# Kernel tuning notes

Hardware: AMD Instinct MI355X
Metric: run time of the kernel (lower is better)

## Reference

```python
import jax, jax.numpy as jnp
import numpy as np


def setup_inputs() -> dict:
    key = jax.random.key(0)
    k1, k2 = jax.random.split(key)
    B, N, M, D = 8, 4096, 4096, 3
    return {
        "input": jax.random.normal(k1, (B, N, D), dtype=jnp.float32),
        "target": jax.random.normal(k2, (B, M, D), dtype=jnp.float32),
    }


def reference(input, target):
    x2 = jnp.sum(input * input, axis=-1)          # [B, N]
    y2 = jnp.sum(target * target, axis=-1)        # [B, M]
    xy = jnp.einsum("bnd,bmd->bnm", input, target)  # [B, N, M]
    sqdist = x2[:, :, None] + y2[:, None, :] - 2.0 * xy
    sqdist = jnp.maximum(sqdist, 0.0)  # clamp numerical negatives
    sqdist1 = jnp.min(sqdist, axis=2)  # nearest target for each input point [B, N]
    sqdist2 = jnp.min(sqdist, axis=1)  # nearest input for each target point [B, M]
    return jnp.mean(sqdist1) + jnp.mean(sqdist2)
```

## Files before the change

### kernel.cpp

```cpp
#include <hip/hip_runtime.h>
#include <math.h>

#define BATCH 8
#define NPTS  4096
#define TPB   256
#define NCC   4
#define CHUNK (NPTS / NCC)
#define ROWS  256
#define NRC   (NPTS / ROWS)
#define WROWS 64

typedef __bf16 bf16x8 __attribute__((ext_vector_type(8)));
typedef float  f32x16 __attribute__((ext_vector_type(16)));

__global__ __launch_bounds__(TPB) void chamfer_mfma_kernel(
    const float* __restrict__ input,
    const float* __restrict__ target,
    float* __restrict__ part)
{
  const int dir = blockIdx.z, b = blockIdx.y;
  const int rc = blockIdx.x & (NRC - 1);
  const int cc = blockIdx.x >> 4;

  const float* __restrict__ qp = (dir ? target : input) + (size_t)b * NPTS * 3;
  const float* __restrict__ cp = (dir ? input  : target) + (size_t)b * NPTS * 3;

  __shared__ bf16x8 sB[2][CHUNK];
  __shared__ bf16x8 sA[2][ROWS];

  {
    const int c0 = cc * CHUNK + (int)threadIdx.x * 4;
    const float4* __restrict__ cv = (const float4*)(cp + 3 * c0);
    const float4 f0 = cv[0], f1 = cv[1], f2 = cv[2];
    float xs[4] = { f0.x, f0.w, f1.z, f2.y };
    float ys[4] = { f0.y, f1.x, f1.w, f2.z };
    float zs[4] = { f0.z, f1.y, f2.x, f2.w };
    #pragma unroll
    for (int j = 0; j < 4; ++j) {
      const float mx = -2.f * xs[j], my = -2.f * ys[j], mz = -2.f * zs[j];
      const __bf16 hx = (__bf16)mx, hy = (__bf16)my, hz = (__bf16)mz;
      const __bf16 lx = (__bf16)(mx - (float)hx);
      const __bf16 ly = (__bf16)(my - (float)hy);
      const __bf16 lz = (__bf16)(mz - (float)hz);
      const float y2 = fmaf(xs[j], xs[j], fmaf(ys[j], ys[j], zs[j] * zs[j]));
      const __bf16 h2 = (__bf16)y2, l2 = (__bf16)(y2 - (float)h2);
      const __bf16 z0 = (__bf16)0.f;
      bf16x8 v0, v1;
      v0[0]=hx; v0[1]=hy; v0[2]=hz; v0[3]=lx; v0[4]=ly; v0[5]=lz; v0[6]=z0; v0[7]=z0;
      v1[0]=hx; v1[1]=hy; v1[2]=hz; v1[3]=h2; v1[4]=l2; v1[5]=z0; v1[6]=z0; v1[7]=z0;
      sB[0][threadIdx.x * 4 + j] = v0;
      sB[1][threadIdx.x * 4 + j] = v1;
    }
  }
  {
    const int r = rc * ROWS + (int)threadIdx.x;
    const float qx = qp[3*r], qy = qp[3*r+1], qz = qp[3*r+2];
    const __bf16 hx = (__bf16)qx, hy = (__bf16)qy, hz = (__bf16)qz;
    const __bf16 lx = (__bf16)(qx - (float)hx);
    const __bf16 ly = (__bf16)(qy - (float)hy);
    const __bf16 lz = (__bf16)(qz - (float)hz);
    const __bf16 z0 = (__bf16)0.f, o1 = (__bf16)1.f;
    bf16x8 v0, v1;
    v0[0]=hx; v0[1]=hy; v0[2]=hz; v0[3]=hx; v0[4]=hy; v0[5]=hz; v0[6]=z0; v0[7]=z0;
    v1[0]=lx; v1[1]=ly; v1[2]=lz; v1[3]=o1; v1[4]=o1; v1[5]=z0; v1[6]=z0; v1[7]=z0;
    sA[0][threadIdx.x] = v0;
    sA[1][threadIdx.x] = v1;
  }
  __syncthreads();

  const int lane = (int)threadIdx.x & 63;
  const int wave = (int)threadIdx.x >> 6;
  const int half = lane >> 5;
  const int l31  = lane & 31;

  const bf16x8 a0 = sA[half][wave * WROWS + l31];
  const bf16x8 a1 = sA[half][wave * WROWS + 32 + l31];

  float rm0[16], rm1[16];
  #pragma unroll
  for (int i = 0; i < 16; ++i) { rm0[i] = 3.4e38f; rm1[i] = 3.4e38f; }

  f32x16 zacc;
  #pragma unroll
  for (int i = 0; i < 16; ++i) zacc[i] = 0.f;

  #pragma unroll 2
  for (int m = 0; m < CHUNK / 32; ++m) {
    const bf16x8 bf = sB[half][m * 32 + l31];
    const f32x16 d0 = __builtin_amdgcn_mfma_f32_32x32x16_bf16(a0, bf, zacc, 0, 0, 0);
    const f32x16 d1 = __builtin_amdgcn_mfma_f32_32x32x16_bf16(a1, bf, zacc, 0, 0, 0);
    #pragma unroll
    for (int i = 0; i < 16; ++i) {
      rm0[i] = fminf(rm0[i], d0[i]);
      rm1[i] = fminf(rm1[i], d1[i]);
    }
  }

  float* __restrict__ po = part +
      (((size_t)(dir * BATCH + b) * NCC + cc) * NPTS) + rc * ROWS + wave * WROWS;
  #pragma unroll
  for (int r = 0; r < 16; ++r) {
    float v0 = rm0[r], v1 = rm1[r];
    #pragma unroll
    for (int mk = 1; mk < 32; mk <<= 1) {
      v0 = fminf(v0, __shfl_xor(v0, mk, 64));
      v1 = fminf(v1, __shfl_xor(v1, mk, 64));
    }
    if (l31 == 0) {
      const int row = (r & 3) + 8 * (r >> 2) + 4 * half;
      po[row]      = v0;
      po[row + 32] = v1;
    }
  }
}

__global__ __launch_bounds__(TPB) void chamfer_reduce_kernel(
    const float* __restrict__ part,
    const float* __restrict__ input,
    const float* __restrict__ target,
    float* __restrict__ out)
{
  const int i = (blockIdx.x * TPB + (int)threadIdx.x) * 4;
  const int g = i >> 12;
  const int q = i & (NPTS - 1);
  const int dir = g >> 3, b = g & 7;

  const float* __restrict__ p = part + ((size_t)g * NCC) * NPTS + q;
  float4 mn = *(const float4*)p;
  #pragma unroll
  for (int cc = 1; cc < NCC; ++cc) {
    const float4 t = *(const float4*)(p + (size_t)cc * NPTS);
    mn.x = fminf(mn.x, t.x); mn.y = fminf(mn.y, t.y);
    mn.z = fminf(mn.z, t.z); mn.w = fminf(mn.w, t.w);
  }
  const float* __restrict__ qp =
      (dir ? target : input) + (size_t)b * NPTS * 3 + 3 * q;
  const float4* __restrict__ qv = (const float4*)qp;
  const float4 a = qv[0], c = qv[1], e = qv[2];
  const float x20 = fmaf(a.x, a.x, fmaf(a.y, a.y, a.z * a.z));
  const float x21 = fmaf(a.w, a.w, fmaf(c.x, c.x, c.y * c.y));
  const float x22 = fmaf(c.z, c.z, fmaf(c.w, c.w, e.x * e.x));
  const float x23 = fmaf(e.y, e.y, fmaf(e.z, e.z, e.w * e.w));

  float s = fmaxf(mn.x + x20, 0.f) + fmaxf(mn.y + x21, 0.f) +
            fmaxf(mn.z + x22, 0.f) + fmaxf(mn.w + x23, 0.f);
  #pragma unroll
  for (int off = 32; off > 0; off >>= 1)
    s += __shfl_down(s, off, 64);

  __shared__ float wsum[TPB / 64];
  if ((threadIdx.x & 63) == 0) wsum[threadIdx.x >> 6] = s;
  __syncthreads();
  if (threadIdx.x == 0) {
    const float t = wsum[0] + wsum[1] + wsum[2] + wsum[3];
    atomicAdd(out, t * (1.0f / (float)(BATCH * NPTS)));
  }
}

extern "C" void kernel_launch(void* const* d_in, const int* in_sizes, int n_in,
                              void* d_out, int out_size, void* d_ws, size_t ws_size,
                              hipStream_t stream) {
  const float* input  = (const float*)d_in[0];
  const float* target = (const float*)d_in[1];
  float* out  = (float*)d_out;
  float* part = (float*)d_ws;

  hipMemsetAsync(out, 0, sizeof(float), stream);

  dim3 grid1(NRC * NCC, BATCH, 2);
  chamfer_mfma_kernel<<<grid1, dim3(TPB), 0, stream>>>(input, target, part);

  dim3 grid2((2 * BATCH * NPTS) / (TPB * 4));
  chamfer_reduce_kernel<<<grid2, dim3(TPB), 0, stream>>>(part, input, target, out);
}
```

Measured before the change: 75.33 us.

## Replace shuffle row-min with swizzled LDS transpose and fold norm+clamp into MFMA kernel

```diff
diff --git a/kernel.cpp b/kernel.cpp
--- a/kernel.cpp
+++ b/kernel.cpp
@@ -8,7 +8,6 @@
 #define CHUNK (NPTS / NCC)
 #define ROWS  256
 #define NRC   (NPTS / ROWS)
-#define WROWS 64
 
 typedef __bf16 bf16x8 __attribute__((ext_vector_type(8)));
 typedef float  f32x16 __attribute__((ext_vector_type(16)));
@@ -52,9 +51,10 @@
       sB[1][threadIdx.x * 4 + j] = v1;
     }
   }
+  float qx, qy, qz;
   {
     const int r = rc * ROWS + (int)threadIdx.x;
-    const float qx = qp[3*r], qy = qp[3*r+1], qz = qp[3*r+2];
+    qx = qp[3*r]; qy = qp[3*r+1]; qz = qp[3*r+2];
     const __bf16 hx = (__bf16)qx, hy = (__bf16)qy, hz = (__bf16)qz;
     const __bf16 lx = (__bf16)(qx - (float)hx);
     const __bf16 ly = (__bf16)(qy - (float)hy);
@@ -73,8 +73,8 @@
   const int half = lane >> 5;
   const int l31  = lane & 31;
 
-  const bf16x8 a0 = sA[half][wave * WROWS + l31];
-  const bf16x8 a1 = sA[half][wave * WROWS + 32 + l31];
+  const bf16x8 a0 = sA[half][wave * 64 + l31];
+  const bf16x8 a1 = sA[half][wave * 64 + 32 + l31];
 
   float rm0[16], rm1[16];
   #pragma unroll
@@ -84,66 +84,61 @@
   #pragma unroll
   for (int i = 0; i < 16; ++i) zacc[i] = 0.f;
 
-  #pragma unroll 2
-  for (int m = 0; m < CHUNK / 32; ++m) {
-    const bf16x8 bf = sB[half][m * 32 + l31];
-    const f32x16 d0 = __builtin_amdgcn_mfma_f32_32x32x16_bf16(a0, bf, zacc, 0, 0, 0);
-    const f32x16 d1 = __builtin_amdgcn_mfma_f32_32x32x16_bf16(a1, bf, zacc, 0, 0, 0);
+  #pragma unroll
+  for (int m = 0; m < CHUNK / 32; m += 2) {
+    const bf16x8 bfA = sB[half][m * 32 + l31];
+    const bf16x8 bfB = sB[half][m * 32 + 32 + l31];
+    const f32x16 dA0 = __builtin_amdgcn_mfma_f32_32x32x16_bf16(a0, bfA, zacc, 0, 0, 0);
+    const f32x16 dA1 = __builtin_amdgcn_mfma_f32_32x32x16_bf16(a1, bfA, zacc, 0, 0, 0);
+    const f32x16 dB0 = __builtin_amdgcn_mfma_f32_32x32x16_bf16(a0, bfB, zacc, 0, 0, 0);
+    const f32x16 dB1 = __builtin_amdgcn_mfma_f32_32x32x16_bf16(a1, bfB, zacc, 0, 0, 0);
     #pragma unroll
     for (int i = 0; i < 16; ++i) {
-      rm0[i] = fminf(rm0[i], d0[i]);
-      rm1[i] = fminf(rm1[i], d1[i]);
+      rm0[i] = fminf(fminf(dA0[i], dB0[i]), rm0[i]);
+      rm1[i] = fminf(fminf(dA1[i], dB1[i]), rm1[i]);
     }
   }
 
-  float* __restrict__ po = part +
-      (((size_t)(dir * BATCH + b) * NCC + cc) * NPTS) + rc * ROWS + wave * WROWS;
+  __syncthreads();
+  float* __restrict__ scr = (float*)sB;
   #pragma unroll
   for (int r = 0; r < 16; ++r) {
-    float v0 = rm0[r], v1 = rm1[r];
-    #pragma unroll
-    for (int mk = 1; mk < 32; mk <<= 1) {
-      v0 = fminf(v0, __shfl_xor(v0, mk, 64));
-      v1 = fminf(v1, __shfl_xor(v1, mk, 64));
-    }
-    if (l31 == 0) {
-      const int row = (r & 3) + 8 * (r >> 2) + 4 * half;
-      po[row]      = v0;
-      po[row + 32] = v1;
-    }
+    const int row0 = wave * 64 + (r & 3) + 8 * (r >> 2) + 4 * half;
+    const int sw   = ((row0 & 7) << 2);
+    scr[row0 * 32 + (l31 ^ sw)]        = rm0[r];
+    scr[(row0 + 32) * 32 + (l31 ^ sw)] = rm1[r];
   }
+  __syncthreads();
+
+  const int t = (int)threadIdx.x;
+  const float4* __restrict__ rp = (const float4*)(scr + t * 32);
+  float mn = 3.4e38f;
+  #pragma unroll
+  for (int k = 0; k < 8; ++k) {
+    const float4 v = rp[k ^ (t & 7)];
+    mn = fminf(mn, fminf(fminf(v.x, v.y), fminf(v.z, v.w)));
+  }
+  const float x2 = fmaf(qx, qx, fmaf(qy, qy, qz * qz));
+  part[((size_t)(dir * BATCH + b) * NCC + cc) * NPTS + rc * ROWS + t] =
+      fmaxf(mn + x2, 0.f);
 }
 
 __global__ __launch_bounds__(TPB) void chamfer_reduce_kernel(
-    const float* __restrict__ part,
-    const float* __restrict__ input,
-    const float* __restrict__ target,
-    float* __restrict__ out)
+    const float* __restrict__ part, float* __restrict__ out)
 {
   const int i = (blockIdx.x * TPB + (int)threadIdx.x) * 4;
   const int g = i >> 12;
   const int q = i & (NPTS - 1);
-  const int dir = g >> 3, b = g & 7;
 
   const float* __restrict__ p = part + ((size_t)g * NCC) * NPTS + q;
   float4 mn = *(const float4*)p;
   #pragma unroll
   for (int cc = 1; cc < NCC; ++cc) {
-    const float4 t = *(const float4*)(p + (size_t)cc * NPTS);
-    mn.x = fminf(mn.x, t.x); mn.y = fminf(mn.y, t.y);
-    mn.z = fminf(mn.z, t.z); mn.w = fminf(mn.w, t.w);
+    const float4 v = *(const float4*)(p + (size_t)cc * NPTS);
+    mn.x = fminf(mn.x, v.x); mn.y = fminf(mn.y, v.y);
+    mn.z = fminf(mn.z, v.z); mn.w = fminf(mn.w, v.w);
   }
-  const float* __restrict__ qp =
-      (dir ? target : input) + (size_t)b * NPTS * 3 + 3 * q;
-  const float4* __restrict__ qv = (const float4*)qp;
-  const float4 a = qv[0], c = qv[1], e = qv[2];
-  const float x20 = fmaf(a.x, a.x, fmaf(a.y, a.y, a.z * a.z));
-  const float x21 = fmaf(a.w, a.w, fmaf(c.x, c.x, c.y * c.y));
-  const float x22 = fmaf(c.z, c.z, fmaf(c.w, c.w, e.x * e.x));
-  const float x23 = fmaf(e.y, e.y, fmaf(e.z, e.z, e.w * e.w));
-
-  float s = fmaxf(mn.x + x20, 0.f) + fmaxf(mn.y + x21, 0.f) +
-            fmaxf(mn.z + x22, 0.f) + fmaxf(mn.w + x23, 0.f);
+  float s = mn.x + mn.y + mn.z + mn.w;
   #pragma unroll
   for (int off = 32; off > 0; off >>= 1)
     s += __shfl_down(s, off, 64);
@@ -152,8 +147,8 @@
   if ((threadIdx.x & 63) == 0) wsum[threadIdx.x >> 6] = s;
   __syncthreads();
   if (threadIdx.x == 0) {
-    const float t = wsum[0] + wsum[1] + wsum[2] + wsum[3];
-    atomicAdd(out, t * (1.0f / (float)(BATCH * NPTS)));
+    const float v = wsum[0] + wsum[1] + wsum[2] + wsum[3];
+    atomicAdd(out, v * (1.0f / (float)(BATCH * NPTS)));
   }
 }
 
@@ -171,5 +166,5 @@
   chamfer_mfma_kernel<<<grid1, dim3(TPB), 0, stream>>>(input, target, part);
 
   dim3 grid2((2 * BATCH * NPTS) / (TPB * 4));
-  chamfer_reduce_kernel<<<grid2, dim3(TPB), 0, stream>>>(part, input, target, out);
+  chamfer_reduce_kernel<<<grid2, dim3(TPB), 0, stream>>>(part, out);
 }
```

Measured after the change: 73.80 us, median of 2. 2.0% less time.
